# Kernel optimization log

Measured on AMD Instinct MI355X. Metric: run time of the kernel, lower is better.

## Reference

```python
import jax, jax.numpy as jnp
import numpy as np

B, C, M = 64, 64, 8192
EPS = 1e-05

def setup_inputs() -> dict:
    key = jax.random.key(0)
    x = jax.random.normal(key, (B, C, M), dtype=jnp.float32)
    return {"x": x}

def _mT(a):
    return jnp.swapaxes(a, -1, -2)

def reference(x):
    b, c, m = x.shape
    mu = x.mean(axis=2, keepdims=True)
    xc = x - mu
    cov = (xc @ _mT(xc)) / m                      # (B,C,C)
    # RBLW shrinkage
    I = jnp.eye(c, dtype=x.dtype)[None]
    trace = jnp.trace(cov, axis1=-2, axis2=-1)[:, None, None]
    second_trace = jnp.einsum('bij,bji->b', cov, cov)[:, None, None]
    numerator = (m - 2) / m * second_trace + trace ** 2
    denominator = (m + 2) * (second_trace - trace ** 2 / c)
    rho = jnp.minimum(numerator / denominator, 1.0)
    F_hat = trace / c * I
    cov = rho * F_hat + (1 - rho) * cov + EPS * I
    # eigen decomposition (no-grad in original)
    covs = jax.lax.stop_gradient(cov)
    U, L, _ = jnp.linalg.svd(covs)                # U:(B,C,C) L:(B,C) descending
    ratio = jnp.cumsum(L, axis=1) / jnp.sum(L, axis=1, keepdims=True)
    conds = jnp.any(ratio >= 1 - EPS, axis=0) | jnp.any(L <= EPS, axis=0)  # (C,)
    counter = jnp.where(jnp.any(conds), jnp.argmax(conds), c)
    # iterative rank-1 eigen refinement + deflation via scan with break mask
    Ucols = jnp.moveaxis(U, 2, 0)[..., None]      # (C,B,C,1)
    Lcols = L.T                                    # (C,B)
    S0 = jnp.zeros_like(cov)

    def step(carry, inp):
        cov_c, S_hat, active = carry
        v, Lj, j = inp                            # v:(B,C,1), Lj:(B,)
        step_active = active & (j < counter)
        # power_layer forward is identity on v
        vt = _mT(v)
        lam = (vt @ cov_c @ v) / (vt @ v)         # (B,1,1)
        Lj = Lj[:, None, None]
        ok = step_active & (~jnp.any(lam < 0)) & (~jnp.any(jnp.abs(lam - Lj) / Lj > 0.1))
        lam_safe = jnp.where(ok, lam, jnp.ones_like(lam))
        vvT = v @ vt
        S_hat = S_hat + jnp.where(ok, jax.lax.rsqrt(lam_safe) * vvT, 0.0)
        cov_c = jnp.where(ok, cov_c - cov_c @ vvT, cov_c)
        return (cov_c, S_hat, ok), None

    (_, S_hat, _), _ = jax.lax.scan(step, (cov, S0, jnp.array(True)),
                                    (Ucols, Lcols, jnp.arange(c)))
    Z = S_hat @ xc
    return Z
```

## Files before the change

### kernel.cpp

```cpp
#include <hip/hip_runtime.h>
#include <math.h>

#define BB 64
#define CCH 64
#define MMH 8192
#define SLICES 8
#define KSL 1024
#define KCH 128
#define TNB 128
constexpr double EPSV = 1e-5;

typedef __attribute__((ext_vector_type(8))) short bf16x8;
typedef __attribute__((ext_vector_type(8))) unsigned short u16x8;
typedef __attribute__((ext_vector_type(16))) float floatx16;

__device__ __forceinline__ void split3(float f, unsigned short& q1, unsigned short& q2,
                                       unsigned short& q3) {
  unsigned u = __float_as_uint(f);
  q1 = (unsigned short)(u >> 16);
  float r1 = f - __uint_as_float(u & 0xffff0000u);
  unsigned u1 = __float_as_uint(r1);
  q2 = (unsigned short)(u1 >> 16);
  float r2 = r1 - __uint_as_float(u1 & 0xffff0000u);
  q3 = (unsigned short)(__float_as_uint(r2) >> 16);
}

__global__ __launch_bounds__(256, 3) void k1_partG(const float* __restrict__ x,
                                                   float* __restrict__ Gpart,
                                                   float* __restrict__ rspart) {
  __shared__ unsigned short h1[64][KCH + 8], h2[64][KCH + 8], h3[64][KCH + 8];
  __shared__ float rred[64][4];
  const int tid = threadIdx.x;
  const int b = blockIdx.x / SLICES;
  const int s = blockIdx.x % SLICES;
  const int row = tid >> 2;
  const int seg = (tid & 3) * 32;
  const int wv = tid >> 6;
  const int lane = tid & 63;
  const int rw = wv >> 1, cw = wv & 1;
  const int mrow = 32 * rw + (lane & 31);
  const int ncol = 32 * cw + (lane & 31);
  const int koff = (lane >> 5) * 8;
  const float* xb = x + (size_t)b * CCH * MMH + (size_t)s * KSL;
  floatx16 acc = {};
  float rsum = 0.f;
  for (int c = 0; c < KSL / KCH; ++c) {
    const float* xp = xb + (size_t)row * MMH + c * KCH + seg;
    float v[32];
#pragma unroll
    for (int q = 0; q < 8; ++q) {
      float4 t = *(const float4*)(xp + 4 * q);
      v[4 * q] = t.x;
      v[4 * q + 1] = t.y;
      v[4 * q + 2] = t.z;
      v[4 * q + 3] = t.w;
    }
#pragma unroll
    for (int o = 0; o < 32; ++o) rsum += v[o];
#pragma unroll
    for (int g = 0; g < 4; ++g) {
      u16x8 a1, a2, a3;
#pragma unroll
      for (int j = 0; j < 8; ++j) {
        unsigned short q1, q2, q3;
        split3(v[8 * g + j], q1, q2, q3);
        a1[j] = q1;
        a2[j] = q2;
        a3[j] = q3;
      }
      *(u16x8*)&h1[row][seg + 8 * g] = a1;
      *(u16x8*)&h2[row][seg + 8 * g] = a2;
      *(u16x8*)&h3[row][seg + 8 * g] = a3;
    }
    __syncthreads();
#pragma unroll
    for (int ks = 0; ks < KCH / 16; ++ks) {
      const int kk = ks * 16 + koff;
      bf16x8 A1 = *(const bf16x8*)&h1[mrow][kk];
      bf16x8 A2 = *(const bf16x8*)&h2[mrow][kk];
      bf16x8 A3 = *(const bf16x8*)&h3[mrow][kk];
      bf16x8 B1 = *(const bf16x8*)&h1[ncol][kk];
      bf16x8 B2 = *(const bf16x8*)&h2[ncol][kk];
      bf16x8 B3 = *(const bf16x8*)&h3[ncol][kk];
      acc = __builtin_amdgcn_mfma_f32_32x32x16_bf16(A1, B1, acc, 0, 0, 0);
      acc = __builtin_amdgcn_mfma_f32_32x32x16_bf16(A1, B2, acc, 0, 0, 0);
      acc = __builtin_amdgcn_mfma_f32_32x32x16_bf16(A2, B1, acc, 0, 0, 0);
      acc = __builtin_amdgcn_mfma_f32_32x32x16_bf16(A2, B2, acc, 0, 0, 0);
      acc = __builtin_amdgcn_mfma_f32_32x32x16_bf16(A1, B3, acc, 0, 0, 0);
      acc = __builtin_amdgcn_mfma_f32_32x32x16_bf16(A3, B1, acc, 0, 0, 0);
    }
    __syncthreads();
  }
  float* gp = Gpart + ((size_t)(b * SLICES + s)) * 4096;
#pragma unroll
  for (int r = 0; r < 16; ++r) {
    int row32 = (r & 3) + 8 * (r >> 2) + 4 * (lane >> 5);
    gp[(32 * rw + row32) * 64 + 32 * cw + (lane & 31)] = acc[r];
  }
  rred[row][tid & 3] = rsum;
  __syncthreads();
  if (tid < 64) {
    rspart[((size_t)(b * SLICES + s)) * 64 + tid] =
        rred[tid][0] + rred[tid][1] + rred[tid][2] + rred[tid][3];
  }
}

__global__ __launch_bounds__(256) void k2_reduce(const float* __restrict__ Gpart,
                                                 const float* __restrict__ rspart,
                                                 float* __restrict__ cov32,
                                                 float* __restrict__ mu32,
                                                 double* __restrict__ scal) {
  __shared__ double muS[64];
  __shared__ double red[256];
  const int tid = threadIdx.x;
  const int b = blockIdx.x;
  if (tid < 64) {
    double r = 0.0;
    for (int s = 0; s < SLICES; ++s) r += (double)rspart[((size_t)(b * SLICES + s)) * 64 + tid];
    double mu = r / (double)MMH;
    muS[tid] = mu;
    mu32[b * 64 + tid] = (float)mu;
  }
  __syncthreads();
  const int base = tid * 16;
  const int i = tid >> 2;
  double g[16];
#pragma unroll
  for (int e = 0; e < 16; ++e) g[e] = 0.0;
  for (int s = 0; s < SLICES; ++s) {
    const float* gp = Gpart + ((size_t)(b * SLICES + s)) * 4096 + base;
#pragma unroll
    for (int q = 0; q < 4; ++q) {
      float4 t = *(const float4*)(gp + 4 * q);
      g[4 * q] += (double)t.x;
      g[4 * q + 1] += (double)t.y;
      g[4 * q + 2] += (double)t.z;
      g[4 * q + 3] += (double)t.w;
    }
  }
  double t1 = 0.0, t2 = 0.0;
#pragma unroll
  for (int e = 0; e < 16; ++e) {
    int j = (base + e) & 63;
    double cv = g[e] / (double)MMH - muS[i] * muS[j];
    cov32[(size_t)b * 4096 + base + e] = (float)cv;
    if (i == j) t1 += cv;
    t2 += cv * cv;
  }
  red[tid] = t1;
  __syncthreads();
  for (int st = 128; st > 0; st >>= 1) {
    if (tid < st) red[tid] += red[tid + st];
    __syncthreads();
  }
  double T1 = red[0];
  __syncthreads();
  red[tid] = t2;
  __syncthreads();
  for (int st = 128; st > 0; st >>= 1) {
    if (tid < st) red[tid] += red[tid + st];
    __syncthreads();
  }
  double T2 = red[0];
  if (tid == 0) {
    double num = ((double)(MMH - 2) / (double)MMH) * T2 + T1 * T1;
    double den = (double)(MMH + 2) * (T2 - T1 * T1 / (double)CCH);
    double r = num / den;
    double rho = (r < 1.0) ? r : 1.0;
    scal[b * 4 + 0] = rho;
    scal[b * 4 + 1] = T1 / (double)CCH;
    scal[b * 4 + 2] = 1.0 - rho;
    scal[b * 4 + 3] = (r >= 1.0) ? 1.0 : 0.0;
  }
}

__device__ __forceinline__ void gemm_acc(const float (*A)[64], const float (*B)[64],
                                         int i0, int j0, float acc[4][4]) {
#pragma unroll
  for (int a = 0; a < 4; ++a)
#pragma unroll
    for (int c = 0; c < 4; ++c) acc[a][c] = 0.f;
#pragma unroll 4
  for (int k = 0; k < 64; ++k) {
    const float4 av = *(const float4*)&A[k][i0];
    const float4 bv = *(const float4*)&B[k][j0];
    const float aa[4] = {av.x, av.y, av.z, av.w};
    const float bb[4] = {bv.x, bv.y, bv.z, bv.w};
#pragma unroll
    for (int a = 0; a < 4; ++a)
#pragma unroll
      for (int c = 0; c < 4; ++c) acc[a][c] = fmaf(aa[a], bb[c], acc[a][c]);
  }
}

__global__ __launch_bounds__(256) void k3_eig(const float* __restrict__ cov32,
                                              const double* __restrict__ scal,
                                              const float* __restrict__ mu32,
                                              float* __restrict__ SxG,
                                              float* __restrict__ smuA,
                                              float* __restrict__ vS,
                                              float* __restrict__ wvm) {
  __shared__ float As[64][64];
  __shared__ float Xs[64][64];
  __shared__ float Bs[64][64];
  __shared__ float red[64];
  __shared__ float vSh[64];
  __shared__ float ySh[64];
  __shared__ float muS[64];
  const int tid = threadIdx.x;
  const int b = blockIdx.x & 63;
  const int role = blockIdx.x >> 6;
  const double rho = scal[b * 4 + 0];
  const double alpha0 = scal[b * 4 + 1];
  const int clipped = (scal[b * 4 + 3] != 0.0);
  const float invsqc = (float)(1.0 / sqrt(alpha0 + EPSV));
  const int i0 = (tid >> 4) << 2, j0 = (tid & 15) << 2;
  float acc[4][4];
  if (tid < 64) muS[tid] = mu32[b * 64 + tid];

  if (role == 0) {
    if (clipped) {
      for (int k = tid; k < 4096; k += 256) {
        int i = k >> 6, j = k & 63;
        SxG[(size_t)b * 4096 + k] = (i == j) ? invsqc : 0.f;
      }
      if (tid < 64) smuA[b * 64 + tid] = invsqc * muS[tid];
      return;
    }
    const float orhoc = (float)((1.0 - rho) / (alpha0 + EPSV));
    const float dtermc = (float)((rho * alpha0 + EPSV) / (alpha0 + EPSV));
    for (int k = tid; k < 4096; k += 256) {
      int i = k >> 6, j = k & 63;
      float a = cov32[(size_t)b * 4096 + k];
      As[i][j] = a;
      float t = orhoc * a + ((i == j) ? dtermc : 0.f);
      Xs[i][j] = ((i == j) ? 1.5f : 0.f) - 0.5f * t;
    }
    __syncthreads();
    for (int it = 0; it < 4; ++it) {
      gemm_acc(Xs, Xs, i0, j0, acc);
#pragma unroll
      for (int a = 0; a < 4; ++a)
#pragma unroll
        for (int c = 0; c < 4; ++c) Bs[i0 + a][j0 + c] = acc[a][c];
      __syncthreads();
      gemm_acc(As, Bs, i0, j0, acc);
      float bold[4][4];
#pragma unroll
      for (int a = 0; a < 4; ++a)
#pragma unroll
        for (int c = 0; c < 4; ++c) bold[a][c] = Bs[i0 + a][j0 + c];
      __syncthreads();
#pragma unroll
      for (int a = 0; a < 4; ++a)
#pragma unroll
        for (int c = 0; c < 4; ++c) Bs[i0 + a][j0 + c] = orhoc * acc[a][c] + dtermc * bold[a][c];
      __syncthreads();
      gemm_acc(Xs, Bs, i0, j0, acc);
      float xold[4][4];
#pragma unroll
      for (int a = 0; a < 4; ++a)
#pragma unroll
        for (int c = 0; c < 4; ++c) xold[a][c] = Xs[i0 + a][j0 + c];
      __syncthreads();
#pragma unroll
      for (int a = 0; a < 4; ++a)
#pragma unroll
        for (int c = 0; c < 4; ++c) Xs[i0 + a][j0 + c] = 1.5f * xold[a][c] - 0.5f * acc[a][c];
      __syncthreads();
    }
    for (int k = tid; k < 4096; k += 256) SxG[(size_t)b * 4096 + k] = Xs[k >> 6][k & 63] * invsqc;
    if (tid < 64) {
      float sm = 0.f;
      for (int j = 0; j < 64; ++j) sm += Xs[j][tid] * muS[j];
      smuA[b * 64 + tid] = sm * invsqc;
    }
  } else {
    if (clipped) {
      if (tid < 64) vS[b * 64 + tid] = (tid == 63) ? 1.f : 0.f;
      if (tid == 0) {
        wvm[b * 2] = invsqc;
        wvm[b * 2 + 1] = mu32[b * 64 + 63];
      }
      return;
    }
    for (int k = tid; k < 4096; k += 256) As[k >> 6][k & 63] = cov32[(size_t)b * 4096 + k];
    __syncthreads();
    if (tid < 64) {
      float s = 0.f;
      for (int j = 0; j < 64; ++j) {
        float v = As[j][tid];
        s += (j == tid) ? v : fabsf(v);
      }
      red[tid] = s;
    }
    __syncthreads();
    float sig = 0.f;
    for (int j = 0; j < 64; ++j) sig = fmaxf(sig, red[j]);
    __syncthreads();
#pragma unroll
    for (int a = 0; a < 4; ++a)
#pragma unroll
      for (int c = 0; c < 4; ++c) {
        int i = i0 + a, j = j0 + c;
        Bs[i][j] = ((i == j) ? sig : 0.f) - As[i][j];
      }
    if (i0 == j0)
      red[tid >> 4] = Bs[i0][j0] + Bs[i0 + 1][j0 + 1] + Bs[i0 + 2][j0 + 2] + Bs[i0 + 3][j0 + 3];
    __syncthreads();
    for (int s5 = 0; s5 < 18; ++s5) {
      float t = 0.f;
      for (int j = 0; j < 16; ++j) t += red[j];
      float scale = 1.f / (t * t);
      gemm_acc(Bs, Bs, i0, j0, acc);
      __syncthreads();
#pragma unroll
      for (int a = 0; a < 4; ++a)
#pragma unroll
        for (int c = 0; c < 4; ++c) Bs[i0 + a][j0 + c] = acc[a][c] * scale;
      if (i0 == j0)
        red[tid >> 4] = (acc[0][0] + acc[1][1] + acc[2][2] + acc[3][3]) * scale;
      __syncthreads();
    }
    int jstar = 0;
    float best = -1.f;
    for (int j = 0; j < 64; ++j) {
      float d = Bs[j][j];
      if (d > best) {
        best = d;
        jstar = j;
      }
    }
    if (tid < 64) vSh[tid] = Bs[jstar][tid];
    __syncthreads();
    if (tid < 64) {
      float s = 0.f;
      for (int j = 0; j < 64; ++j) s += As[j][tid] * vSh[j];
      ySh[tid] = s;
    }
    __syncthreads();
    float vy = 0.f, vv = 0.f;
    for (int j = 0; j < 64; ++j) {
      vy += vSh[j] * ySh[j];
      vv += vSh[j] * vSh[j];
    }
    float lam = vy / vv;
    float lampr = (float)(rho * alpha0 + EPSV) + (float)(1.0 - rho) * lam;
    float w = 1.f / sqrtf(lampr);
    float invn = 1.f / sqrtf(vv);
    if (tid < 64) vS[b * 64 + tid] = vSh[tid] * invn;
    if (tid == 0) {
      float vmu = 0.f;
      for (int j = 0; j < 64; ++j) vmu += vSh[j] * invn * muS[j];
      wvm[b * 2] = w;
      wvm[b * 2 + 1] = vmu;
    }
  }
}

__global__ __launch_bounds__(256, 4) void k7_z(const float* __restrict__ x,
                                               const float* __restrict__ SxG,
                                               const float* __restrict__ smuA,
                                               const float* __restrict__ vS,
                                               const float* __restrict__ wvm,
                                               float* __restrict__ z) {
  __shared__ unsigned short S1[64][80], S2[64][80], S3[64][80];
  __shared__ float vsh[64];
  __shared__ float smsh[64];
  const int tid = threadIdx.x;
  const int b = blockIdx.y;
  const int t0 = blockIdx.x * TNB;
  const float w = wvm[b * 2], vmu = wvm[b * 2 + 1];
  if (tid < 64) vsh[tid] = vS[b * 64 + tid];
  __syncthreads();
  {
    const int i = tid >> 2, js = (tid & 3) * 16;
    const float wvi = w * vsh[i];
    const float* sp = SxG + (size_t)b * 4096 + i * 64 + js;
#pragma unroll
    for (int e = 0; e < 16; ++e) {
      float sv = sp[e] - wvi * vsh[js + e];
      unsigned short q1, q2, q3;
      split3(sv, q1, q2, q3);
      S1[i][js + e] = q1;
      S2[i][js + e] = q2;
      S3[i][js + e] = q3;
    }
  }
  if (tid < 64) smsh[tid] = smuA[b * 64 + tid] - w * vsh[tid] * vmu;
  __syncthreads();
  const int wv = tid >> 6, lane = tid & 63;
  const int arow = lane & 31;
  const int krow = (lane >> 5) * 8;
  const int col0 = t0 + wv * 32 + (lane & 31);
  const float* xb = x + (size_t)b * CCH * MMH;
  floatx16 acc0 = {}, acc1 = {};
#pragma unroll
  for (int ks = 0; ks < 4; ++ks) {
    const int kb = ks * 16 + krow;
    float r0[8];
#pragma unroll
    for (int j = 0; j < 8; ++j) r0[j] = xb[(size_t)(kb + j) * MMH + col0];
    bf16x8 B1, B2, B3;
#pragma unroll
    for (int j = 0; j < 8; ++j) {
      unsigned short q1, q2, q3;
      split3(r0[j], q1, q2, q3);
      B1[j] = (short)q1;
      B2[j] = (short)q2;
      B3[j] = (short)q3;
    }
    bf16x8 A1a = *(const bf16x8*)&S1[arow][kb];
    bf16x8 A2a = *(const bf16x8*)&S2[arow][kb];
    bf16x8 A3a = *(const bf16x8*)&S3[arow][kb];
    bf16x8 A1b = *(const bf16x8*)&S1[arow + 32][kb];
    bf16x8 A2b = *(const bf16x8*)&S2[arow + 32][kb];
    bf16x8 A3b = *(const bf16x8*)&S3[arow + 32][kb];
    acc0 = __builtin_amdgcn_mfma_f32_32x32x16_bf16(A1a, B1, acc0, 0, 0, 0);
    acc0 = __builtin_amdgcn_mfma_f32_32x32x16_bf16(A1a, B2, acc0, 0, 0, 0);
    acc0 = __builtin_amdgcn_mfma_f32_32x32x16_bf16(A2a, B1, acc0, 0, 0, 0);
    acc0 = __builtin_amdgcn_mfma_f32_32x32x16_bf16(A2a, B2, acc0, 0, 0, 0);
    acc0 = __builtin_amdgcn_mfma_f32_32x32x16_bf16(A1a, B3, acc0, 0, 0, 0);
    acc0 = __builtin_amdgcn_mfma_f32_32x32x16_bf16(A3a, B1, acc0, 0, 0, 0);
    acc1 = __builtin_amdgcn_mfma_f32_32x32x16_bf16(A1b, B1, acc1, 0, 0, 0);
    acc1 = __builtin_amdgcn_mfma_f32_32x32x16_bf16(A1b, B2, acc1, 0, 0, 0);
    acc1 = __builtin_amdgcn_mfma_f32_32x32x16_bf16(A2b, B1, acc1, 0, 0, 0);
    acc1 = __builtin_amdgcn_mfma_f32_32x32x16_bf16(A2b, B2, acc1, 0, 0, 0);
    acc1 = __builtin_amdgcn_mfma_f32_32x32x16_bf16(A1b, B3, acc1, 0, 0, 0);
    acc1 = __builtin_amdgcn_mfma_f32_32x32x16_bf16(A3b, B1, acc1, 0, 0, 0);
  }
#pragma unroll
  for (int r = 0; r < 16; ++r) {
    const int grow = (r & 3) + 8 * (r >> 2) + 4 * (lane >> 5);
    z[((size_t)b * CCH + grow) * MMH + col0] = acc0[r] - smsh[grow];
    z[((size_t)b * CCH + grow + 32) * MMH + col0] = acc1[r] - smsh[grow + 32];
  }
}

extern "C" void kernel_launch(void* const* d_in, const int* in_sizes, int n_in,
                              void* d_out, int out_size, void* d_ws, size_t ws_size,
                              hipStream_t stream) {
  (void)in_sizes;
  (void)n_in;
  (void)out_size;
  (void)ws_size;
  const float* x = (const float*)d_in[0];
  float* z = (float*)d_out;
  float* Gpart = (float*)d_out;
  float* rspart = (float*)((char*)d_out + 8388608);
  char* ws = (char*)d_ws;
  float* cov32 = (float*)(ws + 0);
  float* mu32 = (float*)(ws + 1048576);
  double* scal = (double*)(ws + 1064960);
  float* SxG = (float*)(ws + 1067008);
  float* smuA = (float*)(ws + 2115584);
  float* vS = (float*)(ws + 2131968);
  float* wvm = (float*)(ws + 2148352);

  k1_partG<<<dim3(BB * SLICES), dim3(256), 0, stream>>>(x, Gpart, rspart);
  k2_reduce<<<dim3(BB), dim3(256), 0, stream>>>(Gpart, rspart, cov32, mu32, scal);
  k3_eig<<<dim3(2 * BB), dim3(256), 0, stream>>>(cov32, scal, mu32, SxG, smuA, vS, wvm);
  k7_z<<<dim3(MMH / TNB, BB), dim3(256), 0, stream>>>(x, SxG, smuA, vS, wvm, z);
}
```

Measured before the change: 317.1 us.

## Fuse covariance reduction into eig kernel and use split-bf16 MFMA for small GEMMs

```diff
diff --git a/kernel.cpp b/kernel.cpp
--- a/kernel.cpp
+++ b/kernel.cpp
@@ -23,6 +23,33 @@
   q2 = (unsigned short)(u1 >> 16);
   float r2 = r1 - __uint_as_float(u1 & 0xffff0000u);
   q3 = (unsigned short)(__float_as_uint(r2) >> 16);
+}
+
+__device__ __forceinline__ floatx16 mm6(const unsigned short (*P1)[72],
+                                        const unsigned short (*P2)[72],
+                                        const unsigned short (*P3)[72],
+                                        const unsigned short (*Q1)[72],
+                                        const unsigned short (*Q2)[72],
+                                        const unsigned short (*Q3)[72],
+                                        int mrow, int ncol, int koff) {
+  floatx16 acc = {};
+#pragma unroll
+  for (int ks = 0; ks < 4; ++ks) {
+    const int kk = ks * 16 + koff;
+    bf16x8 A1 = *(const bf16x8*)&P1[mrow][kk];
+    bf16x8 A2 = *(const bf16x8*)&P2[mrow][kk];
+    bf16x8 A3 = *(const bf16x8*)&P3[mrow][kk];
+    bf16x8 B1 = *(const bf16x8*)&Q1[ncol][kk];
+    bf16x8 B2 = *(const bf16x8*)&Q2[ncol][kk];
+    bf16x8 B3 = *(const bf16x8*)&Q3[ncol][kk];
+    acc = __builtin_amdgcn_mfma_f32_32x32x16_bf16(A1, B1, acc, 0, 0, 0);
+    acc = __builtin_amdgcn_mfma_f32_32x32x16_bf16(A1, B2, acc, 0, 0, 0);
+    acc = __builtin_amdgcn_mfma_f32_32x32x16_bf16(A2, B1, acc, 0, 0, 0);
+    acc = __builtin_amdgcn_mfma_f32_32x32x16_bf16(A2, B2, acc, 0, 0, 0);
+    acc = __builtin_amdgcn_mfma_f32_32x32x16_bf16(A1, B3, acc, 0, 0, 0);
+    acc = __builtin_amdgcn_mfma_f32_32x32x16_bf16(A3, B1, acc, 0, 0, 0);
+  }
+  return acc;
 }
 
 __global__ __launch_bounds__(256, 3) void k1_partG(const float* __restrict__ x,
@@ -105,97 +132,8 @@
   }
 }
 
-__global__ __launch_bounds__(256) void k2_reduce(const float* __restrict__ Gpart,
-                                                 const float* __restrict__ rspart,
-                                                 float* __restrict__ cov32,
-                                                 float* __restrict__ mu32,
-                                                 double* __restrict__ scal) {
-  __shared__ double muS[64];
-  __shared__ double red[256];
-  const int tid = threadIdx.x;
-  const int b = blockIdx.x;
-  if (tid < 64) {
-    double r = 0.0;
-    for (int s = 0; s < SLICES; ++s) r += (double)rspart[((size_t)(b * SLICES + s)) * 64 + tid];
-    double mu = r / (double)MMH;
-    muS[tid] = mu;
-    mu32[b * 64 + tid] = (float)mu;
-  }
-  __syncthreads();
-  const int base = tid * 16;
-  const int i = tid >> 2;
-  double g[16];
-#pragma unroll
-  for (int e = 0; e < 16; ++e) g[e] = 0.0;
-  for (int s = 0; s < SLICES; ++s) {
-    const float* gp = Gpart + ((size_t)(b * SLICES + s)) * 4096 + base;
-#pragma unroll
-    for (int q = 0; q < 4; ++q) {
-      float4 t = *(const float4*)(gp + 4 * q);
-      g[4 * q] += (double)t.x;
-      g[4 * q + 1] += (double)t.y;
-      g[4 * q + 2] += (double)t.z;
-      g[4 * q + 3] += (double)t.w;
-    }
-  }
-  double t1 = 0.0, t2 = 0.0;
-#pragma unroll
-  for (int e = 0; e < 16; ++e) {
-    int j = (base + e) & 63;
-    double cv = g[e] / (double)MMH - muS[i] * muS[j];
-    cov32[(size_t)b * 4096 + base + e] = (float)cv;
-    if (i == j) t1 += cv;
-    t2 += cv * cv;
-  }
-  red[tid] = t1;
-  __syncthreads();
-  for (int st = 128; st > 0; st >>= 1) {
-    if (tid < st) red[tid] += red[tid + st];
-    __syncthreads();
-  }
-  double T1 = red[0];
-  __syncthreads();
-  red[tid] = t2;
-  __syncthreads();
-  for (int st = 128; st > 0; st >>= 1) {
-    if (tid < st) red[tid] += red[tid + st];
-    __syncthreads();
-  }
-  double T2 = red[0];
-  if (tid == 0) {
-    double num = ((double)(MMH - 2) / (double)MMH) * T2 + T1 * T1;
-    double den = (double)(MMH + 2) * (T2 - T1 * T1 / (double)CCH);
-    double r = num / den;
-    double rho = (r < 1.0) ? r : 1.0;
-    scal[b * 4 + 0] = rho;
-    scal[b * 4 + 1] = T1 / (double)CCH;
-    scal[b * 4 + 2] = 1.0 - rho;
-    scal[b * 4 + 3] = (r >= 1.0) ? 1.0 : 0.0;
-  }
-}
-
-__device__ __forceinline__ void gemm_acc(const float (*A)[64], const float (*B)[64],
-                                         int i0, int j0, float acc[4][4]) {
-#pragma unroll
-  for (int a = 0; a < 4; ++a)
-#pragma unroll
-    for (int c = 0; c < 4; ++c) acc[a][c] = 0.f;
-#pragma unroll 4
-  for (int k = 0; k < 64; ++k) {
-    const float4 av = *(const float4*)&A[k][i0];
-    const float4 bv = *(const float4*)&B[k][j0];
-    const float aa[4] = {av.x, av.y, av.z, av.w};
-    const float bb[4] = {bv.x, bv.y, bv.z, bv.w};
-#pragma unroll
-    for (int a = 0; a < 4; ++a)
-#pragma unroll
-      for (int c = 0; c < 4; ++c) acc[a][c] = fmaf(aa[a], bb[c], acc[a][c]);
-  }
-}
-
-__global__ __launch_bounds__(256) void k3_eig(const float* __restrict__ cov32,
-                                              const double* __restrict__ scal,
-                                              const float* __restrict__ mu32,
+__global__ __launch_bounds__(256) void k3_eig(const float* __restrict__ Gpart,
+                                              const float* __restrict__ rspart,
                                               float* __restrict__ SxG,
                                               float* __restrict__ smuA,
                                               float* __restrict__ vS,
@@ -203,20 +141,89 @@
   __shared__ float As[64][64];
   __shared__ float Xs[64][64];
   __shared__ float Bs[64][64];
+  __shared__ unsigned short Pa1[64][72], Pa2[64][72], Pa3[64][72];
+  __shared__ unsigned short Pp1[64][72], Pp2[64][72], Pp3[64][72];
+  __shared__ unsigned short Pq1[64][72], Pq2[64][72], Pq3[64][72];
+  __shared__ double redd[256];
+  __shared__ double muS[64];
+  __shared__ double sc[3];
+  __shared__ float muF[64];
   __shared__ float red[64];
+  __shared__ float redt[2];
   __shared__ float vSh[64];
   __shared__ float ySh[64];
-  __shared__ float muS[64];
   const int tid = threadIdx.x;
   const int b = blockIdx.x & 63;
   const int role = blockIdx.x >> 6;
-  const double rho = scal[b * 4 + 0];
-  const double alpha0 = scal[b * 4 + 1];
-  const int clipped = (scal[b * 4 + 3] != 0.0);
+
+  if (tid < 64) {
+    double r = 0.0;
+    for (int s = 0; s < SLICES; ++s) r += (double)rspart[((size_t)(b * SLICES + s)) * 64 + tid];
+    double mu = r / (double)MMH;
+    muS[tid] = mu;
+    muF[tid] = (float)mu;
+  }
+  __syncthreads();
+  {
+    const int base = tid * 16;
+    const int ii = tid >> 2;
+    double g[16];
+#pragma unroll
+    for (int e = 0; e < 16; ++e) g[e] = 0.0;
+    for (int s = 0; s < SLICES; ++s) {
+      const float* gp = Gpart + ((size_t)(b * SLICES + s)) * 4096 + base;
+#pragma unroll
+      for (int q = 0; q < 4; ++q) {
+        float4 t = *(const float4*)(gp + 4 * q);
+        g[4 * q] += (double)t.x;
+        g[4 * q + 1] += (double)t.y;
+        g[4 * q + 2] += (double)t.z;
+        g[4 * q + 3] += (double)t.w;
+      }
+    }
+    double t1 = 0.0, t2 = 0.0;
+#pragma unroll
+    for (int e = 0; e < 16; ++e) {
+      int j = (base + e) & 63;
+      double cv = g[e] / (double)MMH - muS[ii] * muS[j];
+      As[ii][(tid & 3) * 16 + e] = (float)cv;
+      if (ii == j) t1 += cv;
+      t2 += cv * cv;
+    }
+    redd[tid] = t1;
+    __syncthreads();
+    for (int st = 128; st > 0; st >>= 1) {
+      if (tid < st) redd[tid] += redd[tid + st];
+      __syncthreads();
+    }
+    double T1 = redd[0];
+    __syncthreads();
+    redd[tid] = t2;
+    __syncthreads();
+    for (int st = 128; st > 0; st >>= 1) {
+      if (tid < st) redd[tid] += redd[tid + st];
+      __syncthreads();
+    }
+    double T2 = redd[0];
+    if (tid == 0) {
+      double num = ((double)(MMH - 2) / (double)MMH) * T2 + T1 * T1;
+      double den = (double)(MMH + 2) * (T2 - T1 * T1 / (double)CCH);
+      double r = num / den;
+      sc[0] = (r < 1.0) ? r : 1.0;
+      sc[1] = T1 / (double)CCH;
+      sc[2] = (r >= 1.0) ? 1.0 : 0.0;
+    }
+  }
+  __syncthreads();
+  const double rho = sc[0];
+  const double alpha0 = sc[1];
+  const int clipped = (sc[2] != 0.0);
   const float invsqc = (float)(1.0 / sqrt(alpha0 + EPSV));
-  const int i0 = (tid >> 4) << 2, j0 = (tid & 15) << 2;
-  float acc[4][4];
-  if (tid < 64) muS[tid] = mu32[b * 64 + tid];
+  const int wv = tid >> 6, lane = tid & 63;
+  const int rw = wv >> 1, cw = wv & 1;
+  const int mrow = 32 * rw + (lane & 31);
+  const int ncol = 32 * cw + (lane & 31);
+  const int koff = (lane >> 5) * 8;
 
   if (role == 0) {
     if (clipped) {
@@ -224,55 +231,73 @@
         int i = k >> 6, j = k & 63;
         SxG[(size_t)b * 4096 + k] = (i == j) ? invsqc : 0.f;
       }
-      if (tid < 64) smuA[b * 64 + tid] = invsqc * muS[tid];
+      if (tid < 64) smuA[b * 64 + tid] = invsqc * muF[tid];
       return;
     }
     const float orhoc = (float)((1.0 - rho) / (alpha0 + EPSV));
     const float dtermc = (float)((rho * alpha0 + EPSV) / (alpha0 + EPSV));
     for (int k = tid; k < 4096; k += 256) {
-      int i = k >> 6, j = k & 63;
-      float a = cov32[(size_t)b * 4096 + k];
-      As[i][j] = a;
-      float t = orhoc * a + ((i == j) ? dtermc : 0.f);
-      Xs[i][j] = ((i == j) ? 1.5f : 0.f) - 0.5f * t;
+      int ii = k >> 6, jj = k & 63;
+      float a = As[ii][jj];
+      unsigned short q1, q2, q3;
+      split3(a, q1, q2, q3);
+      Pa1[ii][jj] = q1;
+      Pa2[ii][jj] = q2;
+      Pa3[ii][jj] = q3;
+      float t = orhoc * a + ((ii == jj) ? dtermc : 0.f);
+      Xs[ii][jj] = ((ii == jj) ? 1.5f : 0.f) - 0.5f * t;
     }
     __syncthreads();
     for (int it = 0; it < 4; ++it) {
-      gemm_acc(Xs, Xs, i0, j0, acc);
-#pragma unroll
-      for (int a = 0; a < 4; ++a)
-#pragma unroll
-        for (int c = 0; c < 4; ++c) Bs[i0 + a][j0 + c] = acc[a][c];
-      __syncthreads();
-      gemm_acc(As, Bs, i0, j0, acc);
-      float bold[4][4];
-#pragma unroll
-      for (int a = 0; a < 4; ++a)
-#pragma unroll
-        for (int c = 0; c < 4; ++c) bold[a][c] = Bs[i0 + a][j0 + c];
-      __syncthreads();
-#pragma unroll
-      for (int a = 0; a < 4; ++a)
-#pragma unroll
-        for (int c = 0; c < 4; ++c) Bs[i0 + a][j0 + c] = orhoc * acc[a][c] + dtermc * bold[a][c];
-      __syncthreads();
-      gemm_acc(Xs, Bs, i0, j0, acc);
-      float xold[4][4];
-#pragma unroll
-      for (int a = 0; a < 4; ++a)
-#pragma unroll
-        for (int c = 0; c < 4; ++c) xold[a][c] = Xs[i0 + a][j0 + c];
-      __syncthreads();
-#pragma unroll
-      for (int a = 0; a < 4; ++a)
-#pragma unroll
-        for (int c = 0; c < 4; ++c) Xs[i0 + a][j0 + c] = 1.5f * xold[a][c] - 0.5f * acc[a][c];
+      for (int k = tid; k < 4096; k += 256) {
+        int ii = k >> 6, jj = k & 63;
+        unsigned short q1, q2, q3;
+        split3(Xs[ii][jj], q1, q2, q3);
+        Pp1[ii][jj] = q1;
+        Pp2[ii][jj] = q2;
+        Pp3[ii][jj] = q3;
+      }
+      __syncthreads();
+      floatx16 acc = mm6(Pp1, Pp2, Pp3, Pp1, Pp2, Pp3, mrow, ncol, koff);
+      floatx16 ureg = acc;
+#pragma unroll
+      for (int r = 0; r < 16; ++r) {
+        int row32 = (r & 3) + 8 * (r >> 2) + 4 * (lane >> 5);
+        int gr = 32 * rw + row32, gc = 32 * cw + (lane & 31);
+        unsigned short q1, q2, q3;
+        split3(acc[r], q1, q2, q3);
+        Pq1[gr][gc] = q1;
+        Pq2[gr][gc] = q2;
+        Pq3[gr][gc] = q3;
+      }
+      __syncthreads();
+      acc = mm6(Pa1, Pa2, Pa3, Pq1, Pq2, Pq3, mrow, ncol, koff);
+      __syncthreads();
+#pragma unroll
+      for (int r = 0; r < 16; ++r) {
+        int row32 = (r & 3) + 8 * (r >> 2) + 4 * (lane >> 5);
+        int gr = 32 * rw + row32, gc = 32 * cw + (lane & 31);
+        float v = orhoc * acc[r] + dtermc * ureg[r];
+        unsigned short q1, q2, q3;
+        split3(v, q1, q2, q3);
+        Pq1[gr][gc] = q1;
+        Pq2[gr][gc] = q2;
+        Pq3[gr][gc] = q3;
+      }
+      __syncthreads();
+      acc = mm6(Pp1, Pp2, Pp3, Pq1, Pq2, Pq3, mrow, ncol, koff);
+#pragma unroll
+      for (int r = 0; r < 16; ++r) {
+        int row32 = (r & 3) + 8 * (r >> 2) + 4 * (lane >> 5);
+        int gr = 32 * rw + row32, gc = 32 * cw + (lane & 31);
+        Xs[gr][gc] = 1.5f * Xs[gr][gc] - 0.5f * acc[r];
+      }
       __syncthreads();
     }
     for (int k = tid; k < 4096; k += 256) SxG[(size_t)b * 4096 + k] = Xs[k >> 6][k & 63] * invsqc;
     if (tid < 64) {
       float sm = 0.f;
-      for (int j = 0; j < 64; ++j) sm += Xs[j][tid] * muS[j];
+      for (int j = 0; j < 64; ++j) sm += Xs[j][tid] * muF[j];
       smuA[b * 64 + tid] = sm * invsqc;
     }
   } else {
@@ -280,12 +305,10 @@
       if (tid < 64) vS[b * 64 + tid] = (tid == 63) ? 1.f : 0.f;
       if (tid == 0) {
         wvm[b * 2] = invsqc;
-        wvm[b * 2 + 1] = mu32[b * 64 + 63];
+        wvm[b * 2 + 1] = muF[63];
       }
       return;
     }
-    for (int k = tid; k < 4096; k += 256) As[k >> 6][k & 63] = cov32[(size_t)b * 4096 + k];
-    __syncthreads();
     if (tid < 64) {
       float s = 0.f;
       for (int j = 0; j < 64; ++j) {
@@ -298,28 +321,57 @@
     float sig = 0.f;
     for (int j = 0; j < 64; ++j) sig = fmaxf(sig, red[j]);
     __syncthreads();
-#pragma unroll
-    for (int a = 0; a < 4; ++a)
-#pragma unroll
-      for (int c = 0; c < 4; ++c) {
-        int i = i0 + a, j = j0 + c;
-        Bs[i][j] = ((i == j) ? sig : 0.f) - As[i][j];
-      }
-    if (i0 == j0)
-      red[tid >> 4] = Bs[i0][j0] + Bs[i0 + 1][j0 + 1] + Bs[i0 + 2][j0 + 2] + Bs[i0 + 3][j0 + 3];
+    {
+      const int i0 = (tid >> 4) << 2, j0 = (tid & 15) << 2;
+#pragma unroll
+      for (int a = 0; a < 4; ++a)
+#pragma unroll
+        for (int c = 0; c < 4; ++c) {
+          int i = i0 + a, j = j0 + c;
+          float bv = ((i == j) ? sig : 0.f) - As[i][j];
+          Bs[i][j] = bv;
+          unsigned short q1, q2, q3;
+          split3(bv, q1, q2, q3);
+          Pp1[i][j] = q1;
+          Pp2[i][j] = q2;
+          Pp3[i][j] = q3;
+        }
+    }
+    __syncthreads();
+    if (tid == 0) {
+      float t = 0.f;
+      for (int j = 0; j < 64; ++j) t += Bs[j][j];
+      redt[0] = t;
+      redt[1] = 0.f;
+    }
     __syncthreads();
     for (int s5 = 0; s5 < 18; ++s5) {
-      float t = 0.f;
-      for (int j = 0; j < 16; ++j) t += red[j];
+      float t = redt[0] + redt[1];
       float scale = 1.f / (t * t);
-      gemm_acc(Bs, Bs, i0, j0, acc);
-      __syncthreads();
-#pragma unroll
-      for (int a = 0; a < 4; ++a)
-#pragma unroll
-        for (int c = 0; c < 4; ++c) Bs[i0 + a][j0 + c] = acc[a][c] * scale;
-      if (i0 == j0)
-        red[tid >> 4] = (acc[0][0] + acc[1][1] + acc[2][2] + acc[3][3]) * scale;
+      floatx16 acc = mm6(Pp1, Pp2, Pp3, Pp1, Pp2, Pp3, mrow, ncol, koff);
+      float dsum = 0.f;
+      if (rw == cw) {
+#pragma unroll
+        for (int r = 0; r < 16; ++r) {
+          int row32 = (r & 3) + 8 * (r >> 2) + 4 * (lane >> 5);
+          if (row32 == (lane & 31)) dsum += acc[r];
+        }
+      }
+      for (int off = 32; off > 0; off >>= 1) dsum += __shfl_down(dsum, off);
+      __syncthreads();
+      if (rw == cw && lane == 0) redt[rw] = dsum * scale;
+#pragma unroll
+      for (int r = 0; r < 16; ++r) {
+        int row32 = (r & 3) + 8 * (r >> 2) + 4 * (lane >> 5);
+        int gr = 32 * rw + row32, gc = 32 * cw + (lane & 31);
+        float nv = acc[r] * scale;
+        Bs[gr][gc] = nv;
+        unsigned short q1, q2, q3;
+        split3(nv, q1, q2, q3);
+        Pp1[gr][gc] = q1;
+        Pp2[gr][gc] = q2;
+        Pp3[gr][gc] = q3;
+      }
       __syncthreads();
     }
     int jstar = 0;
@@ -351,7 +403,7 @@
     if (tid < 64) vS[b * 64 + tid] = vSh[tid] * invn;
     if (tid == 0) {
       float vmu = 0.f;
-      for (int j = 0; j < 64; ++j) vmu += vSh[j] * invn * muS[j];
+      for (int j = 0; j < 64; ++j) vmu += vSh[j] * invn * muF[j];
       wvm[b * 2] = w;
       wvm[b * 2 + 1] = vmu;
     }
@@ -449,16 +501,12 @@
   float* Gpart = (float*)d_out;
   float* rspart = (float*)((char*)d_out + 8388608);
   char* ws = (char*)d_ws;
-  float* cov32 = (float*)(ws + 0);
-  float* mu32 = (float*)(ws + 1048576);
-  double* scal = (double*)(ws + 1064960);
-  float* SxG = (float*)(ws + 1067008);
-  float* smuA = (float*)(ws + 2115584);
-  float* vS = (float*)(ws + 2131968);
-  float* wvm = (float*)(ws + 2148352);
+  float* SxG = (float*)(ws + 0);
+  float* smuA = (float*)(ws + 1048576);
+  float* vS = (float*)(ws + 1064960);
+  float* wvm = (float*)(ws + 1081344);
 
   k1_partG<<<dim3(BB * SLICES), dim3(256), 0, stream>>>(x, Gpart, rspart);
-  k2_reduce<<<dim3(BB), dim3(256), 0, stream>>>(Gpart, rspart, cov32, mu32, scal);
-  k3_eig<<<dim3(2 * BB), dim3(256), 0, stream>>>(cov32, scal, mu32, SxG, smuA, vS, wvm);
+  k3_eig<<<dim3(2 * BB), dim3(256), 0, stream>>>(Gpart, rspart, SxG, smuA, vS, wvm);
   k7_z<<<dim3(MMH / TNB, BB), dim3(256), 0, stream>>>(x, SxG, smuA, vS, wvm, z);
 }
```

Result: faster. 295.6 us (-6.8%).
